# Optimization experiments

Hardware: AMD Instinct MI355X
Metric: run time of the kernel (lower is better)

## Reference

```python
import jax, jax.numpy as jnp
from jax import lax
import numpy as np

# pywt sym4 analysis filters (pywt.Wavelet('sym4').dec_lo / .dec_hi)
DEC_LO = np.array([-0.07576571478927333, -0.02963552764599851, 0.49761866763201545,
                   0.8037387518059161, 0.29785779560527736, -0.09921954357684722,
                   -0.012603967262037833, 0.0322231006040427], dtype=np.float32)
DEC_HI = np.array([-0.0322231006040427, -0.012603967262037833, 0.09921954357684722,
                   0.29785779560527736, -0.8037387518059161, 0.49761866763201545,
                   0.02963552764599851, -0.07576571478927333], dtype=np.float32)
L = 8            # sym4 filter length
LEVEL = 4
THRESH = 10.0


def _conv1d(x, kernel, stride, pad):
    # x: (B, T), kernel: (L,) used in correlation sense by lax.conv
    y = lax.conv_general_dilated(x[:, None, :], kernel[None, None, :],
                                 window_strides=(stride,), padding=[pad],
                                 dimension_numbers=('NCH', 'OIH', 'NCH'))
    return y[:, 0, :]


def _dwt1(x, filt):
    # pywt single-level DWT, mode='symmetric':
    #   pad L-1 each side (half-sample symmetric), true convolution, take odd-index
    #   outputs of the 'valid' part -> length floor((N+L-1)/2)
    ext = jnp.pad(x, ((0, 0), (L - 1, L - 1)), mode='symmetric')[:, 1:]
    return _conv1d(ext, filt[::-1], 2, (0, 0))  # flip -> true convolution


def _idwt1(cA, cD, lo, hi):
    # pywt single-level IDWT: upsample by 2, full-convolve with rec filters, sum,
    # trim L-2 from the left, output length 2*n - L + 2.
    B, n = cA.shape
    upA = jnp.zeros((B, 2 * n), cA.dtype).at[:, ::2].set(cA)
    upD = jnp.zeros((B, 2 * n), cD.dtype).at[:, ::2].set(cD)
    # rec_lo = dec_lo[::-1]; full conv w/ rec_lo == correlation w/ dec_lo
    y = _conv1d(upA, lo, 1, (L - 1, L - 1)) + _conv1d(upD, hi, 1, (L - 1, L - 1))
    return y[:, L - 2: L - 2 + 2 * n - L + 2]


def _wavelet_denoise(x):
    lo = jnp.asarray(DEC_LO)
    hi = jnp.asarray(DEC_HI)
    a = x
    details = []
    for _ in range(LEVEL):
        details.append(_dwt1(a, hi))
        a = _dwt1(a, lo)
    # hard threshold: KEEP coefficients with |c| <= threshold, zero the rest
    details = [jnp.where(jnp.abs(d) <= THRESH, d, jnp.zeros_like(d)) for d in details]
    rec = a
    for d in reversed(details):
        if rec.shape[1] > d.shape[1]:     # pywt waverec a[:-1] trim
            rec = rec[:, :d.shape[1]]
        rec = _idwt1(rec, d, lo, hi)
    return rec


def setup_inputs() -> dict:
    key = jax.random.key(0)
    k1, k2 = jax.random.split(key)
    x = jax.random.normal(k1, (100000, 512), dtype=jnp.float32) * 20.0
    edge_index = jax.random.randint(k2, (2, 100000), 0, 100000, dtype=jnp.int64)
    return {"x": x, "edge_index": edge_index, "num_nodes": 100000}


def reference(x, edge_index, num_nodes):
    # edge_index / num_nodes are unused by the original forward
    return _wavelet_denoise(x)
```

## Files before the change

kernel.cpp:

```cpp
#include <hip/hip_runtime.h>
#include <cstddef>

typedef float f2 __attribute__((ext_vector_type(2)));

#define THRESH_V 10.0f
#define RPB 4
#define SLICE 1064

static __device__ __forceinline__ void wave_sync() {
  asm volatile("s_waitcnt lgkmcnt(0)" ::: "memory");
}

#define L0 (-0.07576571478927333f)
#define L1 (-0.02963552764599851f)
#define L2 ( 0.49761866763201545f)
#define L3 ( 0.8037387518059161f)
#define L4 ( 0.29785779560527736f)
#define L5 (-0.09921954357684722f)
#define L6 (-0.012603967262037833f)
#define L7 ( 0.0322231006040427f)
#define H0 (-0.0322231006040427f)
#define H1 (-0.012603967262037833f)
#define H2 ( 0.09921954357684722f)
#define H3 ( 0.29785779560527736f)
#define H4 (-0.8037387518059161f)
#define H5 ( 0.49761866763201545f)
#define H6 ( 0.02963552764599851f)
#define H7 (-0.07576571478927333f)

static __device__ __forceinline__ void fill_ext(float* E, float* O, int n, int lane) {
  int k = 0;
  bool act = false;
  if (lane < 6)                      { k = -1 - lane;      act = true; }
  else if (lane >= 8 && lane < 15)   { k = n + (lane - 8); act = true; }
  if (act) {
    const int src = (k < 0) ? (-1 - k) : (2 * n - 1 - k);
    const float v = (src & 1) ? O[src >> 1] : E[src >> 1];
    if (k & 1) O[(k - 1) >> 1] = v;
    else       E[k >> 1] = v;
  }
}

template <bool SPLIT_OUT>
static __device__ __forceinline__ void fwd_stage(const float* __restrict__ E,
                                                 const float* __restrict__ O,
                                                 int n,
                                                 float* __restrict__ caE,
                                                 float* __restrict__ caO,
                                                 float* __restrict__ cd,
                                                 int lane) {
#pragma clang fp contract(off)
  const f2 CLa = {L7, L5}, CLb = {L6, L4}, CLc = {L3, L1}, CLd = {L2, L0};
  const f2 CHa = {H7, H5}, CHb = {H6, H4}, CHc = {H3, H1}, CHd = {H2, H0};
  const int m = (n + 7) >> 1;
  float* const myCa = SPLIT_OUT ? ((lane & 1) ? caO : caE) : caE;
  for (int i = lane; i < m; i += 64) {
    const float* e = E + i - 3;
    const float* o = O + i - 3;
    f2 Ea; Ea.x = e[0]; Ea.y = e[1];
    f2 Eb; Eb.x = e[2]; Eb.y = e[3];
    f2 Oa; Oa.x = o[0]; Oa.y = o[1];
    f2 Ob; Ob.x = o[2]; Ob.y = o[3];
    f2 t1 = Ea * CLa + Oa * CLb;
    f2 t2 = Eb * CLc + Ob * CLd;
    const float sLo = (t1.x + t1.y) + (t2.x + t2.y);
    f2 s1 = Ea * CHa + Oa * CHb;
    f2 s2 = Eb * CHc + Ob * CHd;
    const float sHi = (s1.x + s1.y) + (s2.x + s2.y);
    if constexpr (SPLIT_OUT) myCa[i >> 1] = sLo;
    else                     caE[i] = sLo;
    cd[i] = (fabsf(sHi) <= THRESH_V) ? sHi : 0.f;
  }
}

static __device__ __forceinline__ void inv_stage(const float* __restrict__ ca,
                                                 const float* __restrict__ cd,
                                                 float* __restrict__ dst,
                                                 int outLen, int lane) {
#pragma clang fp contract(fast)
  const f2 SEa = {L1, L3}, SEb = {L5, L7}, SEc = {H1, H3}, SEd = {H5, H7};
  const f2 SOa = {L0, L2}, SOb = {L4, L6}, SOc = {H0, H2}, SOd = {H4, H6};
  const int pairs = (outLen + 1) >> 1;
  for (int t = lane; t < pairs; t += 64) {
    f2 a01; a01.x = ca[t];     a01.y = ca[t + 1];
    f2 a23; a23.x = ca[t + 2]; a23.y = ca[t + 3];
    f2 d01; d01.x = cd[t];     d01.y = cd[t + 1];
    f2 d23; d23.x = cd[t + 2]; d23.y = cd[t + 3];
    f2 mE = a01 * SEa + a23 * SEb + d01 * SEc + d23 * SEd;
    f2 mO = a01 * SOa + a23 * SOb + d01 * SOc + d23 * SOd;
    const float se = mE.x + mE.y;
    const float so = mO.x + mO.y;
    const int q = 2 * t;
    if (q + 1 < outLen) {
      f2 r; r.x = se; r.y = so;
      *reinterpret_cast<f2*>(dst + q) = r;
    } else {
      dst[q] = se;
    }
  }
}

__global__ __launch_bounds__(256, 8) void wavelet_denoise_kernel(
    const float* __restrict__ x, float* __restrict__ out, int nrows) {
  __shared__ float lds[RPB][SLICE];
  const int wave = threadIdx.x >> 6;
  const int lane = threadIdx.x & 63;
  const int row = blockIdx.x * RPB + wave;
  if (row >= nrows) return;

  float* S = lds[wave];
  float* sxE  = S + 4;    float* sxO  = S + 268;
  float* ca1E = S + 532;  float* ca1O = S + 670;
  float* d1   = S + 804;
  float* ca2E = S + 4;    float* ca2O = S + 78;
  float* d2   = S + 148;
  float* ca3E = S + 286;  float* ca3O = S + 330;
  float* d3   = S + 368;
  float* ca4  = S + 438;  float* d4   = S + 476;
  float* rec70  = S + 528;
  float* rec133 = S + 0;
  float* rec259 = S + 528;

  {
    const float4* src4 = reinterpret_cast<const float4*>(x + (size_t)row * 512);
    f2* dE = reinterpret_cast<f2*>(sxE);
    f2* dO = reinterpret_cast<f2*>(sxO);
    for (int c = lane; c < 128; c += 64) {
      float4 v = src4[c];
      f2 a; a.x = v.x; a.y = v.z;
      f2 b; b.x = v.y; b.y = v.w;
      dE[c] = a;
      dO[c] = b;
    }
  }
  wave_sync();
  fill_ext(sxE, sxO, 512, lane);
  wave_sync();

  fwd_stage<true >(sxE,  sxO,  512, ca1E, ca1O,   d1, lane); wave_sync();
  fill_ext(ca1E, ca1O, 259, lane);                           wave_sync();
  fwd_stage<true >(ca1E, ca1O, 259, ca2E, ca2O,   d2, lane); wave_sync();
  fill_ext(ca2E, ca2O, 133, lane);                           wave_sync();
  fwd_stage<true >(ca2E, ca2O, 133, ca3E, ca3O,   d3, lane); wave_sync();
  fill_ext(ca3E, ca3O, 70, lane);                            wave_sync();
  fwd_stage<false>(ca3E, ca3O,  70, ca4,  nullptr, d4, lane); wave_sync();

  inv_stage(ca4,    d4, rec70,   70, lane); wave_sync();
  inv_stage(rec70,  d3, rec133, 133, lane); wave_sync();
  inv_stage(rec133, d2, rec259, 259, lane); wave_sync();
  inv_stage(rec259, d1, out + (size_t)row * 512, 512, lane);
}

extern "C" void kernel_launch(void* const* d_in, const int* in_sizes, int n_in,
                              void* d_out, int out_size, void* d_ws, size_t ws_size,
                              hipStream_t stream) {
  const float* x = (const float*)d_in[0];
  float* out = (float*)d_out;
  const int nrows = in_sizes[0] / 512;
  const int grid = (nrows + RPB - 1) / RPB;
  wavelet_denoise_kernel<<<dim3(grid), dim3(256), 0, stream>>>(x, out, nrows);
}
```

Measured before the change: 346.9 us.

## Process two rows per wave with interleaved float2 LDS layout and fp16 level-1 details

```diff
diff --git a/kernel.cpp b/kernel.cpp
--- a/kernel.cpp
+++ b/kernel.cpp
@@ -2,153 +2,180 @@
 #include <cstddef>
 
 typedef float f2 __attribute__((ext_vector_type(2)));
+typedef float f4 __attribute__((ext_vector_type(4)));
+typedef _Float16 h2 __attribute__((ext_vector_type(2)));
 
 #define THRESH_V 10.0f
-#define RPB 4
-#define SLICE 1064
+#define WPB 2
+#define SLICE_F2 930
 
 static __device__ __forceinline__ void wave_sync() {
   asm volatile("s_waitcnt lgkmcnt(0)" ::: "memory");
 }
 
-#define L0 (-0.07576571478927333f)
-#define L1 (-0.02963552764599851f)
-#define L2 ( 0.49761866763201545f)
-#define L3 ( 0.8037387518059161f)
-#define L4 ( 0.29785779560527736f)
-#define L5 (-0.09921954357684722f)
-#define L6 (-0.012603967262037833f)
-#define L7 ( 0.0322231006040427f)
-#define H0 (-0.0322231006040427f)
-#define H1 (-0.012603967262037833f)
-#define H2 ( 0.09921954357684722f)
-#define H3 ( 0.29785779560527736f)
-#define H4 (-0.8037387518059161f)
-#define H5 ( 0.49761866763201545f)
-#define H6 ( 0.02963552764599851f)
-#define H7 (-0.07576571478927333f)
+#define L0f (-0.07576571478927333f)
+#define L1f (-0.02963552764599851f)
+#define L2f ( 0.49761866763201545f)
+#define L3f ( 0.8037387518059161f)
+#define L4f ( 0.29785779560527736f)
+#define L5f (-0.09921954357684722f)
+#define L6f (-0.012603967262037833f)
+#define L7f ( 0.0322231006040427f)
+#define H0f (-0.0322231006040427f)
+#define H1f (-0.012603967262037833f)
+#define H2f ( 0.09921954357684722f)
+#define H3f ( 0.29785779560527736f)
+#define H4f (-0.8037387518059161f)
+#define H5f ( 0.49761866763201545f)
+#define H6f ( 0.02963552764599851f)
+#define H7f (-0.07576571478927333f)
 
-static __device__ __forceinline__ void fill_ext(float* E, float* O, int n, int lane) {
-  int k = 0;
-  bool act = false;
-  if (lane < 6)                      { k = -1 - lane;      act = true; }
-  else if (lane >= 8 && lane < 15)   { k = n + (lane - 8); act = true; }
+static __device__ __forceinline__ void fill_ext(f2* E, f2* O, int n, int lane) {
+  int k = 0; bool act = false;
+  if (lane < 6)                    { k = -1 - lane;      act = true; }
+  else if (lane >= 8 && lane < 15) { k = n + (lane - 8); act = true; }
   if (act) {
     const int src = (k < 0) ? (-1 - k) : (2 * n - 1 - k);
-    const float v = (src & 1) ? O[src >> 1] : E[src >> 1];
+    const f2 v = (src & 1) ? O[src >> 1] : E[src >> 1];
     if (k & 1) O[(k - 1) >> 1] = v;
     else       E[k >> 1] = v;
   }
 }
 
-template <bool SPLIT_OUT>
-static __device__ __forceinline__ void fwd_stage(const float* __restrict__ E,
-                                                 const float* __restrict__ O,
-                                                 int n,
-                                                 float* __restrict__ caE,
-                                                 float* __restrict__ caO,
-                                                 float* __restrict__ cd,
-                                                 int lane) {
+template <bool SPLIT_OUT, bool D16>
+static __device__ __forceinline__ void fwd_stage(const f2* __restrict__ E,
+                                                 const f2* __restrict__ O, int n,
+                                                 f2* __restrict__ caE,
+                                                 f2* __restrict__ caO,
+                                                 void* __restrict__ cdv, int lane) {
 #pragma clang fp contract(off)
-  const f2 CLa = {L7, L5}, CLb = {L6, L4}, CLc = {L3, L1}, CLd = {L2, L0};
-  const f2 CHa = {H7, H5}, CHb = {H6, H4}, CHc = {H3, H1}, CHd = {H2, H0};
   const int m = (n + 7) >> 1;
-  float* const myCa = SPLIT_OUT ? ((lane & 1) ? caO : caE) : caE;
+  f2* const cdf = (f2*)cdv;
+  h2* const cdh = (h2*)cdv;
+  f2* const myCa = SPLIT_OUT ? ((lane & 1) ? caO : caE) : caE;
   for (int i = lane; i < m; i += 64) {
-    const float* e = E + i - 3;
-    const float* o = O + i - 3;
-    f2 Ea; Ea.x = e[0]; Ea.y = e[1];
-    f2 Eb; Eb.x = e[2]; Eb.y = e[3];
-    f2 Oa; Oa.x = o[0]; Oa.y = o[1];
-    f2 Ob; Ob.x = o[2]; Ob.y = o[3];
-    f2 t1 = Ea * CLa + Oa * CLb;
-    f2 t2 = Eb * CLc + Ob * CLd;
-    const float sLo = (t1.x + t1.y) + (t2.x + t2.y);
-    f2 s1 = Ea * CHa + Oa * CHb;
-    f2 s2 = Eb * CHc + Ob * CHd;
-    const float sHi = (s1.x + s1.y) + (s2.x + s2.y);
+    const f2* e = E + i - 3;
+    const f2* o = O + i - 3;
+    f2 v0 = e[0], v2 = e[1], v4 = e[2], v6 = e[3];
+    f2 v1 = o[0], v3 = o[1], v5 = o[2], v7 = o[3];
+    f2 sLo = ((v0 * L7f + v1 * L6f) + (v2 * L5f + v3 * L4f)) +
+             ((v4 * L3f + v5 * L2f) + (v6 * L1f + v7 * L0f));
+    f2 sHi = ((v0 * H7f + v1 * H6f) + (v2 * H5f + v3 * H4f)) +
+             ((v4 * H3f + v5 * H2f) + (v6 * H1f + v7 * H0f));
     if constexpr (SPLIT_OUT) myCa[i >> 1] = sLo;
     else                     caE[i] = sLo;
-    cd[i] = (fabsf(sHi) <= THRESH_V) ? sHi : 0.f;
-  }
-}
-
-static __device__ __forceinline__ void inv_stage(const float* __restrict__ ca,
-                                                 const float* __restrict__ cd,
-                                                 float* __restrict__ dst,
-                                                 int outLen, int lane) {
-#pragma clang fp contract(fast)
-  const f2 SEa = {L1, L3}, SEb = {L5, L7}, SEc = {H1, H3}, SEd = {H5, H7};
-  const f2 SOa = {L0, L2}, SOb = {L4, L6}, SOc = {H0, H2}, SOd = {H4, H6};
-  const int pairs = (outLen + 1) >> 1;
-  for (int t = lane; t < pairs; t += 64) {
-    f2 a01; a01.x = ca[t];     a01.y = ca[t + 1];
-    f2 a23; a23.x = ca[t + 2]; a23.y = ca[t + 3];
-    f2 d01; d01.x = cd[t];     d01.y = cd[t + 1];
-    f2 d23; d23.x = cd[t + 2]; d23.y = cd[t + 3];
-    f2 mE = a01 * SEa + a23 * SEb + d01 * SEc + d23 * SEd;
-    f2 mO = a01 * SOa + a23 * SOb + d01 * SOc + d23 * SOd;
-    const float se = mE.x + mE.y;
-    const float so = mO.x + mO.y;
-    const int q = 2 * t;
-    if (q + 1 < outLen) {
-      f2 r; r.x = se; r.y = so;
-      *reinterpret_cast<f2*>(dst + q) = r;
+    const float dx = (fabsf(sHi.x) <= THRESH_V) ? sHi.x : 0.f;
+    const float dy = (fabsf(sHi.y) <= THRESH_V) ? sHi.y : 0.f;
+    if constexpr (D16) {
+      h2 r; r.x = (_Float16)dx; r.y = (_Float16)dy;
+      cdh[i] = r;
     } else {
-      dst[q] = se;
+      f2 d; d.x = dx; d.y = dy;
+      cdf[i] = d;
     }
   }
 }
 
-__global__ __launch_bounds__(256, 8) void wavelet_denoise_kernel(
+template <bool D16, bool GOUT>
+static __device__ __forceinline__ void inv_stage(const f2* __restrict__ ca,
+                                                 const void* __restrict__ cdv,
+                                                 f2* __restrict__ dst,
+                                                 float* __restrict__ gA,
+                                                 float* __restrict__ gB, bool hasB,
+                                                 int outLen, int lane) {
+#pragma clang fp contract(fast)
+  const f2* const cf = (const f2*)cdv;
+  const h2* const ch = (const h2*)cdv;
+  const int pairs = (outLen + 1) >> 1;
+  for (int t = lane; t < pairs; t += 64) {
+    f2 a0 = ca[t], a1 = ca[t + 1], a2 = ca[t + 2], a3 = ca[t + 3];
+    f2 e0, e1, e2, e3;
+    if constexpr (D16) {
+      h2 x0 = ch[t], x1 = ch[t + 1], x2 = ch[t + 2], x3 = ch[t + 3];
+      e0.x = (float)x0.x; e0.y = (float)x0.y;
+      e1.x = (float)x1.x; e1.y = (float)x1.y;
+      e2.x = (float)x2.x; e2.y = (float)x2.y;
+      e3.x = (float)x3.x; e3.y = (float)x3.y;
+    } else {
+      e0 = cf[t]; e1 = cf[t + 1]; e2 = cf[t + 2]; e3 = cf[t + 3];
+    }
+    f2 se = a0 * L1f + a1 * L3f + a2 * L5f + a3 * L7f +
+            e0 * H1f + e1 * H3f + e2 * H5f + e3 * H7f;
+    f2 so = a0 * L0f + a1 * L2f + a2 * L4f + a3 * L6f +
+            e0 * H0f + e1 * H2f + e2 * H4f + e3 * H6f;
+    const int q = 2 * t;
+    if constexpr (GOUT) {
+      *reinterpret_cast<float2*>(gA + q) = make_float2(se.x, so.x);
+      if (hasB) *reinterpret_cast<float2*>(gB + q) = make_float2(se.y, so.y);
+    } else {
+      if (q + 1 < outLen) {
+        f4 r; r.x = se.x; r.y = se.y; r.z = so.x; r.w = so.y;
+        *reinterpret_cast<f4*>(dst + q) = r;
+      } else {
+        dst[q] = se;
+      }
+    }
+  }
+}
+
+__global__ __launch_bounds__(128, 8) void wavelet_denoise_kernel(
     const float* __restrict__ x, float* __restrict__ out, int nrows) {
-  __shared__ float lds[RPB][SLICE];
+  __shared__ __align__(16) f2 lds[WPB][SLICE_F2];
   const int wave = threadIdx.x >> 6;
   const int lane = threadIdx.x & 63;
-  const int row = blockIdx.x * RPB + wave;
-  if (row >= nrows) return;
+  const int nPairs = (nrows + 1) >> 1;
+  const int pairId = blockIdx.x * WPB + wave;
+  if (pairId >= nPairs) return;
 
-  float* S = lds[wave];
-  float* sxE  = S + 4;    float* sxO  = S + 268;
-  float* ca1E = S + 532;  float* ca1O = S + 670;
-  float* d1   = S + 804;
-  float* ca2E = S + 4;    float* ca2O = S + 78;
-  float* d2   = S + 148;
-  float* ca3E = S + 286;  float* ca3O = S + 330;
-  float* d3   = S + 368;
-  float* ca4  = S + 438;  float* d4   = S + 476;
-  float* rec70  = S + 528;
-  float* rec133 = S + 0;
-  float* rec259 = S + 528;
+  const int rA = 2 * pairId;
+  const bool hasB = (rA + 1) < nrows;
+  const int rBc = hasB ? rA + 1 : rA;
+
+  f2* Sp   = lds[wave];
+  f2* sxE  = Sp + 4;    f2* sxO  = Sp + 268;
+  f2* ca1E = Sp + 531;  f2* ca1O = Sp + 667;
+  h2* d1   = (h2*)(Sp + 800);
+  f2* ca2E = Sp + 4;    f2* ca2O = Sp + 78;
+  f2* d2   = Sp + 148;
+  f2* ca3E = Sp + 286;  f2* ca3O = Sp + 328;
+  f2* d3   = Sp + 366;
+  f2* ca4  = Sp + 436;  f2* d4   = Sp + 474;
+  f2* rec70  = Sp + 528;
+  f2* rec133 = Sp + 0;
+  f2* rec259 = Sp + 528;
 
   {
-    const float4* src4 = reinterpret_cast<const float4*>(x + (size_t)row * 512);
-    f2* dE = reinterpret_cast<f2*>(sxE);
-    f2* dO = reinterpret_cast<f2*>(sxO);
+    const float4* sA4 = reinterpret_cast<const float4*>(x + (size_t)rA * 512);
+    const float4* sB4 = reinterpret_cast<const float4*>(x + (size_t)rBc * 512);
     for (int c = lane; c < 128; c += 64) {
-      float4 v = src4[c];
-      f2 a; a.x = v.x; a.y = v.z;
-      f2 b; b.x = v.y; b.y = v.w;
-      dE[c] = a;
-      dO[c] = b;
+      float4 a = sA4[c];
+      float4 b = sB4[c];
+      f4 ev; ev.x = a.x; ev.y = b.x; ev.z = a.z; ev.w = b.z;
+      f4 ov; ov.x = a.y; ov.y = b.y; ov.z = a.w; ov.w = b.w;
+      *reinterpret_cast<f4*>(sxE + 2 * c) = ev;
+      *reinterpret_cast<f4*>(sxO + 2 * c) = ov;
     }
   }
   wave_sync();
-  fill_ext(sxE, sxO, 512, lane);
+  fill_ext(sxE, sxO, 512, lane); wave_sync();
+
+  fwd_stage<true,  true >(sxE,  sxO,  512, ca1E, ca1O, d1, lane); wave_sync();
+  fill_ext(ca1E, ca1O, 259, lane);                                wave_sync();
+  fwd_stage<true,  false>(ca1E, ca1O, 259, ca2E, ca2O, d2, lane); wave_sync();
+  fill_ext(ca2E, ca2O, 133, lane);                                wave_sync();
+  fwd_stage<true,  false>(ca2E, ca2O, 133, ca3E, ca3O, d3, lane); wave_sync();
+  fill_ext(ca3E, ca3O, 70, lane);                                 wave_sync();
+  fwd_stage<false, false>(ca3E, ca3O, 70, ca4, nullptr, d4, lane); wave_sync();
+
+  float* gA = out + (size_t)rA * 512;
+  float* gB = out + (size_t)rBc * 512;
+  inv_stage<false, false>(ca4,    d4, rec70,  nullptr, nullptr, false,  70, lane);
   wave_sync();
-
-  fwd_stage<true >(sxE,  sxO,  512, ca1E, ca1O,   d1, lane); wave_sync();
-  fill_ext(ca1E, ca1O, 259, lane);                           wave_sync();
-  fwd_stage<true >(ca1E, ca1O, 259, ca2E, ca2O,   d2, lane); wave_sync();
-  fill_ext(ca2E, ca2O, 133, lane);                           wave_sync();
-  fwd_stage<true >(ca2E, ca2O, 133, ca3E, ca3O,   d3, lane); wave_sync();
-  fill_ext(ca3E, ca3O, 70, lane);                            wave_sync();
-  fwd_stage<false>(ca3E, ca3O,  70, ca4,  nullptr, d4, lane); wave_sync();
-
-  inv_stage(ca4,    d4, rec70,   70, lane); wave_sync();
-  inv_stage(rec70,  d3, rec133, 133, lane); wave_sync();
-  inv_stage(rec133, d2, rec259, 259, lane); wave_sync();
-  inv_stage(rec259, d1, out + (size_t)row * 512, 512, lane);
+  inv_stage<false, false>(rec70,  d3, rec133, nullptr, nullptr, false, 133, lane);
+  wave_sync();
+  inv_stage<false, false>(rec133, d2, rec259, nullptr, nullptr, false, 259, lane);
+  wave_sync();
+  inv_stage<true,  true >(rec259, d1, nullptr, gA, gB, hasB, 512, lane);
 }
 
 extern "C" void kernel_launch(void* const* d_in, const int* in_sizes, int n_in,
@@ -157,6 +184,7 @@
   const float* x = (const float*)d_in[0];
   float* out = (float*)d_out;
   const int nrows = in_sizes[0] / 512;
-  const int grid = (nrows + RPB - 1) / RPB;
-  wavelet_denoise_kernel<<<dim3(grid), dim3(256), 0, stream>>>(x, out, nrows);
+  const int nPairs = (nrows + 1) >> 1;
+  const int grid = (nPairs + WPB - 1) / WPB;
+  wavelet_denoise_kernel<<<dim3(grid), dim3(WPB * 64), 0, stream>>>(x, out, nrows);
 }
```

Result: no change. 343.0 us (-1.1%).
